# Optimization experiments

Hardware: AMD Instinct MI355X
Metric: run time of the kernel (lower is better)

## Reference

```python
import jax, jax.numpy as jnp
import numpy as np

N_EMBD = 1024
N_HEAD = 16
HEAD_DIM = N_EMBD // N_HEAD
EPS = 1e-5


def setup_inputs() -> dict:
    key = jax.random.key(0)
    ks = jax.random.split(key, 12)
    C = N_EMBD
    s = lambda fan_in: 1.0 / np.sqrt(fan_in)
    return {
        "x": jax.random.normal(ks[0], (2, 2048, C), dtype=jnp.float32),
        "ln1_g": jnp.ones((C,), jnp.float32),
        "ln1_b": jnp.zeros((C,), jnp.float32),
        "w_attn": jax.random.normal(ks[1], (C, 3 * C), jnp.float32) * s(C),
        "b_attn": jnp.zeros((3 * C,), jnp.float32),
        "w_proj": jax.random.normal(ks[2], (C, C), jnp.float32) * s(C),
        "b_proj": jnp.zeros((C,), jnp.float32),
        "ln2_g": jnp.ones((C,), jnp.float32),
        "ln2_b": jnp.zeros((C,), jnp.float32),
        "w_fc": jax.random.normal(ks[3], (C, 4 * C), jnp.float32) * s(C),
        "b_fc": jnp.zeros((4 * C,), jnp.float32),
        "w_fc2": jax.random.normal(ks[4], (4 * C, C), jnp.float32) * s(4 * C),
        "b_fc2": jnp.zeros((C,), jnp.float32),
    }


def _layernorm(x, g, b):
    mu = jnp.mean(x, axis=-1, keepdims=True)
    var = jnp.mean(jnp.square(x - mu), axis=-1, keepdims=True)
    return (x - mu) * jax.lax.rsqrt(var + EPS) * g + b


def _attention(x, w_attn, b_attn, w_proj, b_proj):
    B, T, C = x.shape
    qkv = x @ w_attn + b_attn  # [B,T,3C]
    q, k, v = jnp.split(qkv, 3, axis=-1)
    # [B,H,T,D]
    reshape = lambda t: t.reshape(B, T, N_HEAD, HEAD_DIM).transpose(0, 2, 1, 3)
    q, k, v = reshape(q), reshape(k), reshape(v)
    scale = HEAD_DIM ** (-0.5)
    att = jnp.einsum("bhqd,bhkd->bhqk", q, k) * scale  # [B,H,T,T]
    mask = jnp.tril(jnp.ones((T, T), dtype=bool))
    att = jnp.where(mask, att, -jnp.inf)
    att = jax.nn.softmax(att, axis=-1)
    y = jnp.einsum("bhqk,bhkd->bhqd", att, v)
    y = y.transpose(0, 2, 1, 3).reshape(B, T, C)
    return y @ w_proj + b_proj


def _mlp(x, w_fc, b_fc, w_fc2, b_fc2):
    h = jax.nn.gelu(x @ w_fc + b_fc, approximate=False)  # nn.GELU default = exact erf
    return h @ w_fc2 + b_fc2


def reference(x, ln1_g, ln1_b, w_attn, b_attn, w_proj, b_proj,
              ln2_g, ln2_b, w_fc, b_fc, w_fc2, b_fc2):
    x = x + _attention(_layernorm(x, ln1_g, ln1_b), w_attn, b_attn, w_proj, b_proj)
    x = x + _mlp(_layernorm(x, ln2_g, ln2_b), w_fc, b_fc, w_fc2, b_fc2)
    return x
```

## Files before the change

kernel.cpp:

```cpp
#include <hip/hip_runtime.h>
#include <hip/hip_bf16.h>
#include <math.h>

typedef __attribute__((ext_vector_type(8))) __bf16 bf16x8;
typedef __attribute__((ext_vector_type(4))) float floatx4;
typedef __attribute__((ext_vector_type(8))) unsigned short ushort8;

#define C_EMBD 1024
#define T_SEQ 2048
#define NH 16
#define HD 64

static __device__ __forceinline__ unsigned short f2b(float f) {
  __hip_bfloat16 h = __float2bfloat16(f);
  unsigned short u;
  __builtin_memcpy(&u, &h, sizeof(u));
  return u;
}
static __device__ __forceinline__ float b2f(unsigned short u) {
  unsigned int b = ((unsigned int)u) << 16;
  float f;
  __builtin_memcpy(&f, &b, sizeof(f));
  return f;
}

static __device__ __forceinline__ void gload16(const void* g, void* l) {
  __builtin_amdgcn_global_load_lds(
      (__attribute__((address_space(1))) void*)(void*)g,
      (__attribute__((address_space(3))) void*)l, 16, 0, 0);
}

static __device__ __forceinline__ floatx4 mfma_bf16(bf16x8 a, bf16x8 b, floatx4 c) {
  return __builtin_amdgcn_mfma_f32_16x16x32_bf16(a, b, c, 0, 0, 0);
}

__global__ __launch_bounds__(256) void wtrans(const float* __restrict__ in,
                                              unsigned short* __restrict__ out,
                                              int K, int N) {
  __shared__ float t[32][33];
  int n0 = blockIdx.x * 32, k0 = blockIdx.y * 32;
  int tx = threadIdx.x & 31, ty = threadIdx.x >> 5;
#pragma unroll
  for (int i = 0; i < 4; i++)
    t[ty + i * 8][tx] = in[(size_t)(k0 + ty + i * 8) * N + n0 + tx];
  __syncthreads();
#pragma unroll
  for (int i = 0; i < 4; i++)
    out[(size_t)(n0 + ty + i * 8) * K + k0 + tx] = f2b(t[tx][ty + i * 8]);
}

__global__ __launch_bounds__(256) void ln_fwd(const float* __restrict__ x,
                                              const float* __restrict__ g,
                                              const float* __restrict__ bta,
                                              unsigned short* __restrict__ out) {
  int row = blockIdx.x;
  int t = threadIdx.x;
  const float4* xr = (const float4*)(x + (size_t)row * C_EMBD);
  float4 v = xr[t];
  float s = v.x + v.y + v.z + v.w;
  float ss = v.x * v.x + v.y * v.y + v.z * v.z + v.w * v.w;
#pragma unroll
  for (int m = 1; m < 64; m <<= 1) {
    s += __shfl_xor(s, m, 64);
    ss += __shfl_xor(ss, m, 64);
  }
  __shared__ float ps[8];
  int wv = t >> 6;
  if ((t & 63) == 0) { ps[wv] = s; ps[4 + wv] = ss; }
  __syncthreads();
  s = ps[0] + ps[1] + ps[2] + ps[3];
  ss = ps[4] + ps[5] + ps[6] + ps[7];
  float mu = s * (1.0f / C_EMBD);
  float var = ss * (1.0f / C_EMBD) - mu * mu;
  float rs = rsqrtf(var + 1e-5f);
  float4 gv = ((const float4*)g)[t];
  float4 bv = ((const float4*)bta)[t];
  ushort4 o;
  o.x = f2b((v.x - mu) * rs * gv.x + bv.x);
  o.y = f2b((v.y - mu) * rs * gv.y + bv.y);
  o.z = f2b((v.z - mu) * rs * gv.z + bv.z);
  o.w = f2b((v.w - mu) * rs * gv.w + bv.w);
  *(ushort4*)(out + (size_t)row * C_EMBD + t * 4) = o;
}

template <int EP>
__global__ __launch_bounds__(256) void gemm_bt(const unsigned short* __restrict__ A,
                                               const unsigned short* __restrict__ Bt,
                                               const float* __restrict__ bias,
                                               void* __restrict__ outv,
                                               unsigned short* __restrict__ vt,
                                               int M, int N, int K) {
  __shared__ __align__(16) unsigned short As[128 * 32];
  __shared__ __align__(16) unsigned short Bs[128 * 32];
  const int tid = threadIdx.x;
  const int wv = tid >> 6, ln = tid & 63;
  const int quad = ln >> 4, l15 = ln & 15;
  const int wm = wv >> 1, wn = wv & 1;
  const int m0 = blockIdx.y * 128, n0 = blockIdx.x * 128;

  floatx4 acc[4][4];
#pragma unroll
  for (int i = 0; i < 4; i++)
#pragma unroll
    for (int j = 0; j < 4; j++) acc[i][j] = (floatx4)0.0f;

  const int rowA = ln >> 2;
  const int koff = (((ln & 3) ^ ((ln >> 3) & 3)) * 8);
  const int swz = (l15 >> 1) & 3;

  for (int k0 = 0; k0 < K; k0 += 32) {
    if (k0) __syncthreads();
#pragma unroll
    for (int hh = 0; hh < 2; ++hh) {
      int r = hh * 64 + wv * 16 + rowA;
      gload16(A + (size_t)(m0 + r) * K + k0 + koff, &As[(hh * 64 + wv * 16) * 32]);
      gload16(Bt + (size_t)(n0 + r) * K + k0 + koff, &Bs[(hh * 64 + wv * 16) * 32]);
    }
    __syncthreads();
    bf16x8 af[4], bfr[4];
#pragma unroll
    for (int mi = 0; mi < 4; mi++)
      af[mi] = *(const bf16x8*)&As[(wm * 64 + mi * 16 + l15) * 32 + (quad ^ swz) * 8];
#pragma unroll
    for (int ni = 0; ni < 4; ni++)
      bfr[ni] = *(const bf16x8*)&Bs[(wn * 64 + ni * 16 + l15) * 32 + (quad ^ swz) * 8];
#pragma unroll
    for (int mi = 0; mi < 4; mi++)
#pragma unroll
      for (int ni = 0; ni < 4; ni++)
        acc[mi][ni] = mfma_bf16(af[mi], bfr[ni], acc[mi][ni]);
  }

#pragma unroll
  for (int mi = 0; mi < 4; mi++) {
#pragma unroll
    for (int ni = 0; ni < 4; ni++) {
      int col = n0 + wn * 64 + ni * 16 + l15;
      int rowb = m0 + wm * 64 + mi * 16 + quad * 4;
      float bc = bias[col];
      if (EP == 2) {
#pragma unroll
        for (int r = 0; r < 4; r++) {
          float v = acc[mi][ni][r] + bc;
          v = 0.5f * v * (1.0f + erff(v * 0.70710678118f));
          ((unsigned short*)outv)[(size_t)(rowb + r) * N + col] = f2b(v);
        }
      } else {
        if (col < 2048) {
#pragma unroll
          for (int r = 0; r < 4; r++)
            ((unsigned short*)outv)[(size_t)(rowb + r) * N + col] =
                f2b(acc[mi][ni][r] + bc);
        } else {
          int dall = col - 2048;
          int hh2 = dall >> 6, dd = dall & 63;
          int bq = rowb >> 11, t0 = rowb & 2047;
          __align__(8) unsigned short pk[4];
#pragma unroll
          for (int r = 0; r < 4; r++) pk[r] = f2b(acc[mi][ni][r] + bc);
          *(ushort4*)&vt[(size_t)((bq * NH + hh2) * HD + dd) * T_SEQ + t0] =
              *(const ushort4*)pk;
        }
      }
    }
  }
}

__global__ __launch_bounds__(512) void gemm_skinny(const unsigned short* __restrict__ A,
                                                   const unsigned short* __restrict__ Bt,
                                                   const float* __restrict__ bias,
                                                   const float* res, float* out,
                                                   int M, int N, int K) {
  __shared__ __align__(16) unsigned short As[4][128 * 32];
  __shared__ __align__(16) unsigned short Bs[4][128 * 32];
  const int tid = threadIdx.x;
  const int wv = tid >> 6, ln = tid & 63;
  const int quad = ln >> 4, l15 = ln & 15;
  const int wm = wv >> 1, wn = wv & 1;
  const int lin = blockIdx.x;
  const int m0 = (lin >> 3) * 128, n0 = (lin & 7) * 128;

  floatx4 acc[2][4];
#pragma unroll
  for (int i = 0; i < 2; i++)
#pragma unroll
    for (int j = 0; j < 4; j++) acc[i][j] = (floatx4)0.0f;

  const int rowA = ln >> 2;
  const int koff = (((ln & 3) ^ ((ln >> 3) & 3)) * 8);
  const int swz = (l15 >> 1) & 3;

  const unsigned short* aseg = A + (size_t)(m0 + wv * 16 + rowA) * K + koff;
  const unsigned short* bseg = Bt + (size_t)(n0 + wv * 16 + rowA) * K + koff;
  const int ldsOff = (wv * 16) * 32;

  const int nIter = K >> 5;
#pragma unroll
  for (int p = 0; p < 3; ++p) {
    gload16(aseg + (p << 5), &As[p][ldsOff]);
    gload16(bseg + (p << 5), &Bs[p][ldsOff]);
  }

  for (int it = 0; it < nIter; ++it) {
    int rem = nIter - 1 - it;
    if (rem >= 2)      asm volatile("s_waitcnt vmcnt(4)" ::: "memory");
    else if (rem == 1) asm volatile("s_waitcnt vmcnt(2)" ::: "memory");
    else               asm volatile("s_waitcnt vmcnt(0)" ::: "memory");
    asm volatile("s_barrier" ::: "memory");
    if (it + 3 < nIter) {
      int k3 = (it + 3) << 5;
      int b3 = (it + 3) & 3;
      gload16(aseg + k3, &As[b3][ldsOff]);
      gload16(bseg + k3, &Bs[b3][ldsOff]);
    }
    const unsigned short* as = As[it & 3];
    const unsigned short* bs = Bs[it & 3];
    bf16x8 af[2], bfr[4];
#pragma unroll
    for (int mi = 0; mi < 2; mi++)
      af[mi] = *(const bf16x8*)&as[(wm * 32 + mi * 16 + l15) * 32 + (quad ^ swz) * 8];
#pragma unroll
    for (int ni = 0; ni < 4; ni++)
      bfr[ni] = *(const bf16x8*)&bs[(wn * 64 + ni * 16 + l15) * 32 + (quad ^ swz) * 8];
#pragma unroll
    for (int mi = 0; mi < 2; mi++)
#pragma unroll
      for (int ni = 0; ni < 4; ni++)
        acc[mi][ni] = mfma_bf16(af[mi], bfr[ni], acc[mi][ni]);
  }

#pragma unroll
  for (int mi = 0; mi < 2; mi++) {
#pragma unroll
    for (int ni = 0; ni < 4; ni++) {
      int col = n0 + wn * 64 + ni * 16 + l15;
      int rowb = m0 + wm * 32 + mi * 16 + quad * 4;
      float bc = bias[col];
#pragma unroll
      for (int r = 0; r < 4; r++) {
        size_t idx = (size_t)(rowb + r) * N + col;
        out[idx] = acc[mi][ni][r] + bc + res[idx];
      }
    }
  }
}

__global__ __launch_bounds__(256) void attn_fwd(const unsigned short* __restrict__ qkv,
                                                const unsigned short* __restrict__ vt,
                                                unsigned short* __restrict__ y) {
  __shared__ __align__(16) unsigned short Ks[64 * 64];
  __shared__ __align__(16) unsigned short Vs[64 * 64];
  __shared__ __align__(16) unsigned short Ps[4 * 16 * 72];
  const int tid = threadIdx.x;
  const int wv = tid >> 6, ln = tid & 63;
  const int quad = ln >> 4, l15 = ln & 15;
  const int pair = blockIdx.x, h = blockIdx.y, b = blockIdx.z;
  unsigned short* Pw = &Ps[wv * 16 * 72];

  const unsigned short* kbase = qkv + (size_t)b * T_SEQ * 3072 + 1024 + h * HD;
  const unsigned short* vbase = vt + (size_t)(b * NH + h) * HD * T_SEQ;

  int koffs[2], voffs[2], ldst[2];
#pragma unroll
  for (int g = 0; g < 2; g++) {
    int S = wv * 128 + g * 64 + ln;
    int r = S >> 3;
    int c = (S & 7) ^ (r & 7);
    koffs[g] = r * 3072 + c * 8;
    voffs[g] = r * T_SEQ + c * 8;
    ldst[g] = wv * 1024 + g * 512;
  }

  for (int ph = 0; ph < 2; ++ph) {
    const int qt = ph ? (31 - pair) : pair;
    const unsigned short* qp =
        qkv + (size_t)(b * T_SEQ + qt * 64 + wv * 16 + l15) * 3072 + h * HD;
    bf16x8 qf[2];
#pragma unroll
    for (int kc = 0; kc < 2; kc++) {
      ushort8 u = *(const ushort8*)(qp + kc * 32 + quad * 8);
      union { ushort8 u; bf16x8 v; } cv;
#pragma unroll
      for (int j = 0; j < 8; j++) cv.u[j] = f2b(b2f(u[j]) * 0.18033688f);
      qf[kc] = cv.v;
    }

    floatx4 o[4];
#pragma unroll
    for (int dt = 0; dt < 4; dt++) o[dt] = (floatx4)0.0f;
    float lacc = 0.0f;

    auto step = [&](int kt, bool diag) {
      __syncthreads();
#pragma unroll
      for (int g = 0; g < 2; g++) {
        gload16(kbase + (size_t)(kt * 64) * 3072 + koffs[g], &Ks[ldst[g]]);
        gload16(vbase + kt * 64 + voffs[g], &Vs[ldst[g]]);
      }
      __syncthreads();

      floatx4 s[4];
#pragma unroll
      for (int nt = 0; nt < 4; nt++) s[nt] = (floatx4)0.0f;
#pragma unroll
      for (int nt = 0; nt < 4; nt++)
#pragma unroll
        for (int kc = 0; kc < 2; kc++) {
          bf16x8 kf = *(const bf16x8*)
              &Ks[(nt * 16 + l15) * 64 + (((kc * 4 + quad) ^ (l15 & 7)) * 8)];
          s[nt] = mfma_bf16(kf, qf[kc], s[nt]);
        }

      float psum = 0.0f;
#pragma unroll
      for (int nt = 0; nt < 4; nt++) {
        __align__(8) unsigned short pk[4];
#pragma unroll
        for (int r = 0; r < 4; r++) {
          float sv = s[nt][r];
          if (diag && (nt * 16 + quad * 4 + r > wv * 16 + l15)) sv = -1e30f;
          float p = exp2f(sv - 12.0f);
          psum += p;
          pk[r] = f2b(p);
        }
        *(ushort4*)&Pw[l15 * 72 + nt * 16 + quad * 4] = *(const ushort4*)pk;
      }
      lacc += psum;

      bf16x8 pf0 = *(const bf16x8*)&Pw[l15 * 72 + quad * 8];
      bf16x8 pf1 = *(const bf16x8*)&Pw[l15 * 72 + 32 + quad * 8];
#pragma unroll
      for (int dt = 0; dt < 4; dt++) {
        bf16x8 vf0 = *(const bf16x8*)
            &Vs[(dt * 16 + l15) * 64 + ((quad ^ (l15 & 7)) * 8)];
        bf16x8 vf1 = *(const bf16x8*)
            &Vs[(dt * 16 + l15) * 64 + (((4 + quad) ^ (l15 & 7)) * 8)];
        o[dt] = mfma_bf16(vf0, pf0, o[dt]);
        o[dt] = mfma_bf16(vf1, pf1, o[dt]);
      }
    };

    for (int kt = 0; kt < qt; ++kt) step(kt, false);
    step(qt, true);

    lacc += __shfl_xor(lacc, 16, 64);
    lacc += __shfl_xor(lacc, 32, 64);
    float rinv = 1.0f / lacc;
#pragma unroll
    for (int dt = 0; dt < 4; dt++) {
      __align__(8) unsigned short ov[4];
#pragma unroll
      for (int r = 0; r < 4; r++) ov[r] = f2b(o[dt][r] * rinv);
      *(ushort4*)&y[(size_t)(b * T_SEQ + qt * 64 + wv * 16 + l15) * C_EMBD +
                    h * HD + dt * 16 + quad * 4] = *(const ushort4*)ov;
    }
  }
}

extern "C" void kernel_launch(void* const* d_in, const int* in_sizes, int n_in,
                              void* d_out, int out_size, void* d_ws, size_t ws_size,
                              hipStream_t stream) {
  (void)in_sizes; (void)n_in; (void)out_size; (void)ws_size;
  const float* x      = (const float*)d_in[0];
  const float* ln1_g  = (const float*)d_in[1];
  const float* ln1_b  = (const float*)d_in[2];
  const float* w_attn = (const float*)d_in[3];
  const float* b_attn = (const float*)d_in[4];
  const float* w_proj = (const float*)d_in[5];
  const float* b_proj = (const float*)d_in[6];
  const float* ln2_g  = (const float*)d_in[7];
  const float* ln2_b  = (const float*)d_in[8];
  const float* w_fc   = (const float*)d_in[9];
  const float* b_fc   = (const float*)d_in[10];
  const float* w_fc2  = (const float*)d_in[11];
  const float* b_fc2  = (const float*)d_in[12];
  float* out = (float*)d_out;

  char* ws = (char*)d_ws;
  unsigned short* wat  = (unsigned short*)ws; ws += (size_t)3072 * 1024 * 2;
  unsigned short* wpt  = (unsigned short*)ws; ws += (size_t)1024 * 1024 * 2;
  unsigned short* wft  = (unsigned short*)ws; ws += (size_t)4096 * 1024 * 2;
  unsigned short* wf2t = (unsigned short*)ws; ws += (size_t)1024 * 4096 * 2;
  unsigned short* xn   = (unsigned short*)ws; ws += (size_t)4096 * 1024 * 2;
  unsigned short* qkv  = (unsigned short*)ws; ws += (size_t)4096 * 3072 * 2;
  unsigned short* yat  = (unsigned short*)ws; ws += (size_t)4096 * 1024 * 2;
  unsigned short* hbuf = (unsigned short*)ws; ws += (size_t)4096 * 4096 * 2;
  unsigned short* vt = hbuf;

  wtrans<<<dim3(3072 / 32, 1024 / 32), 256, 0, stream>>>(w_attn, wat, 1024, 3072);
  wtrans<<<dim3(1024 / 32, 1024 / 32), 256, 0, stream>>>(w_proj, wpt, 1024, 1024);
  wtrans<<<dim3(4096 / 32, 1024 / 32), 256, 0, stream>>>(w_fc, wft, 1024, 4096);
  wtrans<<<dim3(1024 / 32, 4096 / 32), 256, 0, stream>>>(w_fc2, wf2t, 4096, 1024);

  ln_fwd<<<4096, 256, 0, stream>>>(x, ln1_g, ln1_b, xn);
  gemm_bt<3><<<dim3(24, 32), 256, 0, stream>>>(
      xn, wat, b_attn, qkv, vt, 4096, 3072, 1024);
  attn_fwd<<<dim3(16, NH, 2), 256, 0, stream>>>(qkv, vt, yat);
  gemm_skinny<<<dim3(256), 512, 0, stream>>>(
      yat, wpt, b_proj, x, out, 4096, 1024, 1024);
  ln_fwd<<<4096, 256, 0, stream>>>(out, ln2_g, ln2_b, xn);
  gemm_bt<2><<<dim3(32, 32), 256, 0, stream>>>(
      xn, wft, b_fc, hbuf, nullptr, 4096, 4096, 1024);
  gemm_skinny<<<dim3(256), 512, 0, stream>>>(
      hbuf, wf2t, b_fc2, out, out, 4096, 1024, 4096);
}
```

Baseline: 390.2 us.

## Split-K skinny GEMMs with atomic accumulation into residual-initialized output

Rewrites the skinny projection GEMMs as a 2-way split-K kernel. It uses 256-thread blocks, 512 blocks and larger per-wave tiles, and accumulates results with float atomicAdd into an output buffer that a device-to-device copy pre-fills with x, so the residual is added implicitly. The multi-stage async-copy pipeline with four LDS buffers is replaced by a single-buffered load/sync/compute loop. The intent is more blocks for occupancy and no separate residual reads, at the cost of atomic traffic, lost load/compute overlap and nondeterministic summation order.

```diff
diff --git a/kernel.cpp b/kernel.cpp
--- a/kernel.cpp
+++ b/kernel.cpp
@@ -166,23 +166,26 @@
   }
 }
 
-__global__ __launch_bounds__(512) void gemm_skinny(const unsigned short* __restrict__ A,
+__global__ __launch_bounds__(256) void gemm_skinny(const unsigned short* __restrict__ A,
                                                    const unsigned short* __restrict__ Bt,
                                                    const float* __restrict__ bias,
-                                                   const float* res, float* out,
-                                                   int M, int N, int K) {
-  __shared__ __align__(16) unsigned short As[4][128 * 32];
-  __shared__ __align__(16) unsigned short Bs[4][128 * 32];
+                                                   float* out, int M, int N, int K) {
+  __shared__ __align__(16) unsigned short As[128 * 32];
+  __shared__ __align__(16) unsigned short Bs[128 * 32];
   const int tid = threadIdx.x;
   const int wv = tid >> 6, ln = tid & 63;
   const int quad = ln >> 4, l15 = ln & 15;
   const int wm = wv >> 1, wn = wv & 1;
   const int lin = blockIdx.x;
-  const int m0 = (lin >> 3) * 128, n0 = (lin & 7) * 128;
-
-  floatx4 acc[2][4];
-#pragma unroll
-  for (int i = 0; i < 2; i++)
+  const int m0 = (lin & 31) * 128;
+  const int n0 = ((lin >> 5) & 7) * 128;
+  const int kz = lin >> 8;
+  const int Kh = K >> 1;
+  const int kbeg = kz * Kh, kend = kbeg + Kh;
+
+  floatx4 acc[4][4];
+#pragma unroll
+  for (int i = 0; i < 4; i++)
 #pragma unroll
     for (int j = 0; j < 4; j++) acc[i][j] = (floatx4)0.0f;
 
@@ -190,57 +193,39 @@
   const int koff = (((ln & 3) ^ ((ln >> 3) & 3)) * 8);
   const int swz = (l15 >> 1) & 3;
 
-  const unsigned short* aseg = A + (size_t)(m0 + wv * 16 + rowA) * K + koff;
-  const unsigned short* bseg = Bt + (size_t)(n0 + wv * 16 + rowA) * K + koff;
-  const int ldsOff = (wv * 16) * 32;
-
-  const int nIter = K >> 5;
-#pragma unroll
-  for (int p = 0; p < 3; ++p) {
-    gload16(aseg + (p << 5), &As[p][ldsOff]);
-    gload16(bseg + (p << 5), &Bs[p][ldsOff]);
-  }
-
-  for (int it = 0; it < nIter; ++it) {
-    int rem = nIter - 1 - it;
-    if (rem >= 2)      asm volatile("s_waitcnt vmcnt(4)" ::: "memory");
-    else if (rem == 1) asm volatile("s_waitcnt vmcnt(2)" ::: "memory");
-    else               asm volatile("s_waitcnt vmcnt(0)" ::: "memory");
-    asm volatile("s_barrier" ::: "memory");
-    if (it + 3 < nIter) {
-      int k3 = (it + 3) << 5;
-      int b3 = (it + 3) & 3;
-      gload16(aseg + k3, &As[b3][ldsOff]);
-      gload16(bseg + k3, &Bs[b3][ldsOff]);
-    }
-    const unsigned short* as = As[it & 3];
-    const unsigned short* bs = Bs[it & 3];
-    bf16x8 af[2], bfr[4];
-#pragma unroll
-    for (int mi = 0; mi < 2; mi++)
-      af[mi] = *(const bf16x8*)&as[(wm * 32 + mi * 16 + l15) * 32 + (quad ^ swz) * 8];
+  for (int k0 = kbeg; k0 < kend; k0 += 32) {
+    if (k0 != kbeg) __syncthreads();
+#pragma unroll
+    for (int hh = 0; hh < 2; ++hh) {
+      int r = hh * 64 + wv * 16 + rowA;
+      gload16(A + (size_t)(m0 + r) * K + k0 + koff, &As[(hh * 64 + wv * 16) * 32]);
+      gload16(Bt + (size_t)(n0 + r) * K + k0 + koff, &Bs[(hh * 64 + wv * 16) * 32]);
+    }
+    __syncthreads();
+    bf16x8 af[4], bfr[4];
+#pragma unroll
+    for (int mi = 0; mi < 4; mi++)
+      af[mi] = *(const bf16x8*)&As[(wm * 64 + mi * 16 + l15) * 32 + (quad ^ swz) * 8];
 #pragma unroll
     for (int ni = 0; ni < 4; ni++)
-      bfr[ni] = *(const bf16x8*)&bs[(wn * 64 + ni * 16 + l15) * 32 + (quad ^ swz) * 8];
-#pragma unroll
-    for (int mi = 0; mi < 2; mi++)
+      bfr[ni] = *(const bf16x8*)&Bs[(wn * 64 + ni * 16 + l15) * 32 + (quad ^ swz) * 8];
+#pragma unroll
+    for (int mi = 0; mi < 4; mi++)
 #pragma unroll
       for (int ni = 0; ni < 4; ni++)
         acc[mi][ni] = mfma_bf16(af[mi], bfr[ni], acc[mi][ni]);
   }
 
 #pragma unroll
-  for (int mi = 0; mi < 2; mi++) {
+  for (int mi = 0; mi < 4; mi++) {
 #pragma unroll
     for (int ni = 0; ni < 4; ni++) {
       int col = n0 + wn * 64 + ni * 16 + l15;
-      int rowb = m0 + wm * 32 + mi * 16 + quad * 4;
-      float bc = bias[col];
-#pragma unroll
-      for (int r = 0; r < 4; r++) {
-        size_t idx = (size_t)(rowb + r) * N + col;
-        out[idx] = acc[mi][ni][r] + bc + res[idx];
-      }
+      int rowb = m0 + wm * 64 + mi * 16 + quad * 4;
+      float badd = (kz == 0) ? bias[col] : 0.0f;
+#pragma unroll
+      for (int r = 0; r < 4; r++)
+        atomicAdd(&out[(size_t)(rowb + r) * N + col], acc[mi][ni][r] + badd);
     }
   }
 }
@@ -387,6 +372,8 @@
   unsigned short* hbuf = (unsigned short*)ws; ws += (size_t)4096 * 4096 * 2;
   unsigned short* vt = hbuf;
 
+  hipMemcpyAsync(out, x, (size_t)4096 * 1024 * 4, hipMemcpyDeviceToDevice, stream);
+
   wtrans<<<dim3(3072 / 32, 1024 / 32), 256, 0, stream>>>(w_attn, wat, 1024, 3072);
   wtrans<<<dim3(1024 / 32, 1024 / 32), 256, 0, stream>>>(w_proj, wpt, 1024, 1024);
   wtrans<<<dim3(4096 / 32, 1024 / 32), 256, 0, stream>>>(w_fc, wft, 1024, 4096);
@@ -396,11 +383,11 @@
   gemm_bt<3><<<dim3(24, 32), 256, 0, stream>>>(
       xn, wat, b_attn, qkv, vt, 4096, 3072, 1024);
   attn_fwd<<<dim3(16, NH, 2), 256, 0, stream>>>(qkv, vt, yat);
-  gemm_skinny<<<dim3(256), 512, 0, stream>>>(
-      yat, wpt, b_proj, x, out, 4096, 1024, 1024);
+  gemm_skinny<<<dim3(512), 256, 0, stream>>>(
+      yat, wpt, b_proj, out, 4096, 1024, 1024);
   ln_fwd<<<4096, 256, 0, stream>>>(out, ln2_g, ln2_b, xn);
   gemm_bt<2><<<dim3(32, 32), 256, 0, stream>>>(
       xn, wft, b_fc, hbuf, nullptr, 4096, 4096, 1024);
-  gemm_skinny<<<dim3(256), 512, 0, stream>>>(
-      hbuf, wf2t, b_fc2, out, out, 4096, 1024, 4096);
-}
+  gemm_skinny<<<dim3(512), 256, 0, stream>>>(
+      hbuf, wf2t, b_fc2, out, 4096, 1024, 4096);
+}
```

Measured after the change: 398.8 us. 1.02x slower.
